# Kernel optimization log

Measured on AMD Instinct MI355X. Metric: run time of the kernel, lower is better.

The kernel has to match this reference:

```python
import jax, jax.numpy as jnp
import numpy as np

N = 100000          # nodes
E = 1600000         # directed edges (before self-loops)
F_IN = 500          # num_features
HID = 16            # hidden_dim
HEADS = 8
NUM_CLASSES = 10
NEG_SLOPE = 0.2     # PyG GATConv default
BN_EPS = 1e-5


def setup_inputs() -> dict:
    key = jax.random.key(0)
    ks = jax.random.split(key, 20)
    def glorot(k, shape):
        fan = shape[0] + shape[-1]
        return jax.random.normal(k, shape, jnp.float32) * jnp.sqrt(2.0 / fan)
    x = jax.random.normal(ks[0], (N, F_IN), jnp.float32)
    edge_index = jax.random.randint(ks[1], (2, E), 0, N, dtype=jnp.int32)
    inp = {
        'x': x, 'edge_index': edge_index,
        # conv1: F_IN -> HID, 8 heads
        'W1': glorot(ks[2], (F_IN, HEADS * HID)),
        'a1_src': glorot(ks[3], (HEADS, HID)),
        'a1_dst': glorot(ks[4], (HEADS, HID)),
        'b1': jnp.zeros((HEADS * HID,), jnp.float32),
        'g1': jnp.ones((HEADS * HID,), jnp.float32),
        'be1': jnp.zeros((HEADS * HID,), jnp.float32),
        # conv2: 128 -> HID, 8 heads
        'W2': glorot(ks[5], (HEADS * HID, HEADS * HID)),
        'a2_src': glorot(ks[6], (HEADS, HID)),
        'a2_dst': glorot(ks[7], (HEADS, HID)),
        'b2': jnp.zeros((HEADS * HID,), jnp.float32),
        'g2': jnp.ones((HEADS * HID,), jnp.float32),
        'be2': jnp.zeros((HEADS * HID,), jnp.float32),
        # conv3: 128 -> NUM_CLASSES, 1 head
        'W3': glorot(ks[8], (HEADS * HID, NUM_CLASSES)),
        'a3_src': glorot(ks[9], (1, NUM_CLASSES)),
        'a3_dst': glorot(ks[10], (1, NUM_CLASSES)),
        'b3': jnp.zeros((NUM_CLASSES,), jnp.float32),
    }
    return inp


def gat_conv(x, src, dst, W, a_src, a_dst, b, heads, out_ch):
    n = x.shape[0]
    h = (x @ W).reshape(n, heads, out_ch)                      # [N,H,C]
    al_src = jnp.einsum('nhc,hc->nh', h, a_src)                # [N,H]
    al_dst = jnp.einsum('nhc,hc->nh', h, a_dst)                # [N,H]
    e = al_src[src] + al_dst[dst]                              # [E,H]
    e = jnp.where(e > 0, e, NEG_SLOPE * e)                     # LeakyReLU
    # segment softmax over incoming edges of each dst node
    m = jax.ops.segment_max(e, dst, num_segments=n)            # [N,H]
    m = jnp.where(jnp.isfinite(m), m, 0.0)
    p = jnp.exp(e - m[dst])                                    # [E,H]
    denom = jax.ops.segment_sum(p, dst, num_segments=n)        # [N,H]
    alpha = p / jnp.maximum(denom[dst], 1e-16)                 # [E,H]
    msg = h[src] * alpha[:, :, None]                           # [E,H,C]
    out = jax.ops.segment_sum(msg, dst, num_segments=n)        # [N,H,C]
    return out.reshape(n, heads * out_ch) + b


def batch_norm_eval(x, gamma, beta):
    # eval-mode BN with running_mean=0, running_var=1
    return x * (gamma / jnp.sqrt(1.0 + BN_EPS)) + beta


def reference(x, edge_index, W1, a1_src, a1_dst, b1, g1, be1,
              W2, a2_src, a2_dst, b2, g2, be2,
              W3, a3_src, a3_dst, b3):
    loops = jnp.arange(N, dtype=edge_index.dtype)
    src = jnp.concatenate([edge_index[0], loops])
    dst = jnp.concatenate([edge_index[1], loops])
    h = jax.nn.elu(gat_conv(x, src, dst, W1, a1_src, a1_dst, b1, HEADS, HID))
    h = batch_norm_eval(h, g1, be1)
    h = jax.nn.elu(gat_conv(h, src, dst, W2, a2_src, a2_dst, b2, HEADS, HID))
    h = batch_norm_eval(h, g2, be2)
    h = gat_conv(h, src, dst, W3, a3_src, a3_dst, b3, 1, NUM_CLASSES)
    return jax.nn.log_softmax(h, axis=1)
```

## Files before the change

kernel.cpp:

```cpp
#include <hip/hip_runtime.h>
#include <math.h>

#define N_NODES 100000
#define N_EDGES 1600000
#define ET (N_EDGES + N_NODES)
#define F_IN 500
#define D1 128
#define HEADS 8
#define HID 16
#define NCLS 10
#define MAXDEG 64
#define NB 391
#define NSUB 8
#define CAPS 1024
#define CPAD 16

using frag = __attribute__((ext_vector_type(8))) short;
using f4   = __attribute__((ext_vector_type(4))) float;

__device__ __forceinline__ unsigned short f2bf(float x) {
    unsigned u = __float_as_uint(x);
    unsigned r = u + 0x7fff + ((u >> 16) & 1);
    return (unsigned short)(r >> 16);
}
__device__ __forceinline__ unsigned short f2bf_tr(float x) {
    return (unsigned short)(__float_as_uint(x) >> 16);
}
__device__ __forceinline__ float bf2f(unsigned short b) {
    return __uint_as_float(((unsigned)b) << 16);
}
__device__ __forceinline__ float bflo(unsigned u) { return __uint_as_float(u << 16); }
__device__ __forceinline__ float bfhi(unsigned u) { return __uint_as_float(u & 0xffff0000u); }
__device__ __forceinline__ float lrelu(float e) { return (e > 0.f) ? e : 0.2f * e; }

__global__ __launch_bounds__(256) void k_bin(const int* __restrict__ eidx,
                                             int* __restrict__ bincnt,
                                             int* __restrict__ bin) {
    unsigned xcc;
    asm("s_getreg_b32 %0, hwreg(HW_REG_XCC_ID)" : "=s"(xcc));
    int base = blockIdx.x * 1024 + threadIdx.x;
#pragma unroll
    for (int k = 0; k < 4; k++) {
        int i = base + k * 256;
        if (i < ET) {
            int s, d;
            if (i < N_EDGES) { s = eidx[i]; d = eidx[N_EDGES + i]; }
            else             { s = i - N_EDGES; d = s; }
            int sb = (d >> 8) * NSUB + (int)xcc;
            int pos = atomicAdd(&bincnt[sb * CPAD], 1);
            if (pos < CAPS) bin[(size_t)sb * CAPS + pos] = (s << 8) | (d & 255);
        }
    }
}

__global__ __launch_bounds__(256) void k_build(const int* __restrict__ bincnt,
                                               const int* __restrict__ bin,
                                               int* __restrict__ cnt,
                                               int* __restrict__ slots) {
    __shared__ int lcnt[256];
    __shared__ int lsl[256 * MAXDEG];
    const int b   = blockIdx.x;
    const int tid = threadIdx.x;
    lcnt[tid] = 0;
    __syncthreads();
    for (int sub = 0; sub < NSUB; sub++) {
        int sb = b * NSUB + sub;
        int len = min(bincnt[sb * CPAD], CAPS);
        const int* bp = bin + (size_t)sb * CAPS;
        for (int i = tid; i < len; i += 256) {
            int v = bp[i];
            int doff = v & 255;
            int j = atomicAdd(&lcnt[doff], 1);
            if (j < MAXDEG) lsl[doff * MAXDEG + j] = v >> 8;
        }
    }
    __syncthreads();
    int node0 = b * 256;
    int nloc = min(256, N_NODES - node0);
    if (tid < nloc) cnt[node0 + tid] = min(lcnt[tid], MAXDEG);
    int total4 = (nloc * MAXDEG) >> 2;
    int4* dst4 = (int4*)(slots + (size_t)node0 * MAXDEG);
    const int4* src4 = (const int4*)lsl;
    for (int i = tid; i < total4; i += 256) dst4[i] = src4[i];
}

template<int K, int KP>
__global__ __launch_bounds__(256) void k_pack(const float* __restrict__ W,
                                              short* __restrict__ bhi,
                                              short* __restrict__ blo) {
    int t = blockIdx.x * 256 + threadIdx.x;
    if (t >= KP * 128) return;
    int n = t & 127, k = t >> 7;
    float w = (k < K) ? W[k * 128 + n] : 0.f;
    unsigned short h = f2bf(w);
    unsigned short l = f2bf(w - bf2f(h));
    int kt = k >> 5, kq = (k >> 3) & 3, j = k & 7, nt = n >> 4;
    int lane = kq * 16 + (n & 15);
    int idx = ((kt * 8 + nt) * 64 + lane) * 8 + j;
    bhi[idx] = (short)h;
    blo[idx] = (short)l;
}

template<int K, int NSTEP>
__global__ __launch_bounds__(256, 3) void k_mfma_gemm(const float* __restrict__ A,
                                                      const short* __restrict__ Bhi,
                                                      const short* __restrict__ Blo,
                                                      unsigned* __restrict__ hb, int n) {
    __shared__ short Ah[64 * 40];
    __shared__ short Al[64 * 40];
    const int tid  = threadIdx.x;
    const int lane = tid & 63;
    const int w    = tid >> 6;
    const int wm   = w >> 1, wn = w & 1;
    const int r0   = blockIdx.x * 64;

    float4 ld[2];
    auto issue_loads = [&](int k0) {
#pragma unroll
        for (int p = 0; p < 2; p++) {
            int c = tid + p * 256;
            int row = r0 + (c >> 3);
            int kk = k0 + ((c & 7) << 2);
            if (row < n && kk < K) ld[p] = *(const float4*)(A + (size_t)row * K + kk);
            else                   ld[p] = float4{0.f, 0.f, 0.f, 0.f};
        }
    };
    auto stage = [&]() {
#pragma unroll
        for (int p = 0; p < 2; p++) {
            int c = tid + p * 256;
            int row = c >> 3;
            int kc = (c & 7) << 2;
            float4 v = ld[p];
            unsigned short h0 = f2bf(v.x), h1 = f2bf(v.y), h2 = f2bf(v.z), h3 = f2bf(v.w);
            unsigned short q0 = f2bf_tr(v.x - bf2f(h0)), q1 = f2bf_tr(v.y - bf2f(h1));
            unsigned short q2 = f2bf_tr(v.z - bf2f(h2)), q3 = f2bf_tr(v.w - bf2f(h3));
            int off = row * 40 + kc;
            *(uint2*)(&Ah[off]) = uint2{(unsigned)h0 | ((unsigned)h1 << 16),
                                        (unsigned)h2 | ((unsigned)h3 << 16)};
            *(uint2*)(&Al[off]) = uint2{(unsigned)q0 | ((unsigned)q1 << 16),
                                        (unsigned)q2 | ((unsigned)q3 << 16)};
        }
    };

    f4 acc[2][4];
#pragma unroll
    for (int a = 0; a < 2; a++)
#pragma unroll
        for (int b = 0; b < 4; b++) acc[a][b] = f4{0.f, 0.f, 0.f, 0.f};

    issue_loads(0);
    for (int s = 0; s < NSTEP; s++) {
        if (s > 0) __syncthreads();
        stage();
        if (s + 1 < NSTEP) issue_loads((s + 1) * 32);
        __syncthreads();
        frag ahi[2], alo[2];
        const int kb = (lane >> 4) * 8;
#pragma unroll
        for (int mt = 0; mt < 2; mt++) {
            int row = wm * 32 + mt * 16 + (lane & 15);
            ahi[mt] = *(const frag*)(&Ah[row * 40 + kb]);
            alo[mt] = *(const frag*)(&Al[row * 40 + kb]);
        }
#pragma unroll
        for (int nn = 0; nn < 4; nn++) {
            int nt = wn * 4 + nn;
            frag bh = *(const frag*)(Bhi + (((size_t)s * 8 + nt) * 64 + lane) * 8);
            frag bl = *(const frag*)(Blo + (((size_t)s * 8 + nt) * 64 + lane) * 8);
#pragma unroll
            for (int mt = 0; mt < 2; mt++) {
                acc[mt][nn] = __builtin_amdgcn_mfma_f32_16x16x32_bf16(ahi[mt], bh, acc[mt][nn], 0, 0, 0);
                acc[mt][nn] = __builtin_amdgcn_mfma_f32_16x16x32_bf16(ahi[mt], bl, acc[mt][nn], 0, 0, 0);
                acc[mt][nn] = __builtin_amdgcn_mfma_f32_16x16x32_bf16(alo[mt], bh, acc[mt][nn], 0, 0, 0);
            }
        }
    }

#pragma unroll
    for (int mt = 0; mt < 2; mt++) {
        int rowb = r0 + wm * 32 + mt * 16 + (lane >> 4) * 4;
#pragma unroll
        for (int nn = 0; nn < 4; nn++) {
#pragma unroll
            for (int i = 0; i < 4; i++) {
                float v  = acc[mt][nn][i];
                float v2 = __shfl_xor(v, 1);
                int row = rowb + i;
                if (!(lane & 1) && row < n) {
                    unsigned pk = (unsigned)f2bf(v) | ((unsigned)f2bf(v2) << 16);
                    hb[(size_t)row * 64 + wn * 32 + nn * 8 + ((lane & 15) >> 1)] = pk;
                }
            }
        }
    }
}

__global__ __launch_bounds__(256) void k_attn_bf(const unsigned* __restrict__ hb,
                                                 const float* __restrict__ a_src,
                                                 const float* __restrict__ a_dst,
                                                 float* __restrict__ als,
                                                 float* __restrict__ ald, int n) {
    int t = blockIdx.x * blockDim.x + threadIdx.x;
    if (t >= n * 8) return;
    int hd = t & 7;
    const unsigned* hp = hb + (size_t)(t >> 3) * 64 + hd * 8;
    uint4 ua = *(const uint4*)hp;
    uint4 ub = *(const uint4*)(hp + 4);
    unsigned uu[8] = {ua.x, ua.y, ua.z, ua.w, ub.x, ub.y, ub.z, ub.w};
    float s1 = 0.f, s2 = 0.f;
#pragma unroll
    for (int j = 0; j < 8; j++) {
        unsigned u = uu[j];
        float v0 = bflo(u), v1 = bfhi(u);
        s1 += v0 * a_src[hd * 16 + 2 * j] + v1 * a_src[hd * 16 + 2 * j + 1];
        s2 += v0 * a_dst[hd * 16 + 2 * j] + v1 * a_dst[hd * 16 + 2 * j + 1];
    }
    als[t] = s1;
    ald[t] = s2;
}

__global__ __launch_bounds__(256) void k_agg128(const unsigned* __restrict__ hb,
                                                const float* __restrict__ als,
                                                const float* __restrict__ ald,
                                                const int* __restrict__ cnt,
                                                const int* __restrict__ slots,
                                                const float* __restrict__ bias,
                                                const float* __restrict__ gamma,
                                                const float* __restrict__ beta,
                                                float* __restrict__ out, int n) {
    int lane = threadIdx.x & 63;
    int node = __builtin_amdgcn_readfirstlane(blockIdx.x * 4 + (threadIdx.x >> 6));
    if (node >= n) return;
    int head = lane >> 3;
    float aldv = ald[node * 8 + head];
    int deg = min(cnt[node], MAXDEG);
    const int* sl = slots + (long)node * MAXDEG;

    float l = 0.f, accx = 0.f, accy = 0.f;
    int j = 0;
    for (; j + 1 < deg; j += 2) {
        int s0 = sl[j], s1 = sl[j + 1];
        unsigned u0 = hb[(size_t)s0 * 64 + lane];
        unsigned u1 = hb[(size_t)s1 * 64 + lane];
        float p0 = __expf(lrelu(als[s0 * 8 + head] + aldv));
        float p1 = __expf(lrelu(als[s1 * 8 + head] + aldv));
        l += p0 + p1;
        accx += p0 * bflo(u0) + p1 * bflo(u1);
        accy += p0 * bfhi(u0) + p1 * bfhi(u1);
    }
    if (j < deg) {
        int s0 = sl[j];
        unsigned u0 = hb[(size_t)s0 * 64 + lane];
        float p0 = __expf(lrelu(als[s0 * 8 + head] + aldv));
        l += p0;
        accx += p0 * bflo(u0);
        accy += p0 * bfhi(u0);
    }
    float inv = 1.f / fmaxf(l, 1e-16f);
    const float bnr = rsqrtf(1.0f + 1e-5f);
    int c0 = 2 * lane;
    float v0 = accx * inv + bias[c0];
    v0 = (v0 > 0.f) ? v0 : expm1f(v0);
    v0 = v0 * (gamma[c0] * bnr) + beta[c0];
    float v1 = accy * inv + bias[c0 + 1];
    v1 = (v1 > 0.f) ? v1 : expm1f(v1);
    v1 = v1 * (gamma[c0 + 1] * bnr) + beta[c0 + 1];
    out[(long)node * 128 + c0]     = v0;
    out[(long)node * 128 + c0 + 1] = v1;
}

__global__ __launch_bounds__(256) void k_gemm_w3(const float* __restrict__ A,
                                                 const float* __restrict__ W,
                                                 const float* __restrict__ a_src,
                                                 const float* __restrict__ a_dst,
                                                 float* __restrict__ out,
                                                 float* __restrict__ als,
                                                 float* __restrict__ ald, int n) {
    __shared__ float w[D1 * NCLS];
    for (int idx = threadIdx.x; idx < D1 * NCLS; idx += 256) w[idx] = W[idx];
    __syncthreads();
    int node = blockIdx.x * 256 + threadIdx.x;
    if (node >= n) return;
    const float* ar = A + (long)node * D1;
    float acc[NCLS];
#pragma unroll
    for (int cc = 0; cc < NCLS; cc++) acc[cc] = 0.f;
    for (int k = 0; k < D1; k++) {
        float av = ar[k];
#pragma unroll
        for (int cc = 0; cc < NCLS; cc++) acc[cc] = fmaf(av, w[k * NCLS + cc], acc[cc]);
    }
    float s1 = 0.f, s2 = 0.f;
#pragma unroll
    for (int cc = 0; cc < NCLS; cc++) {
        out[(long)node * NCLS + cc] = acc[cc];
        s1 += acc[cc] * a_src[cc];
        s2 += acc[cc] * a_dst[cc];
    }
    als[node] = s1;
    ald[node] = s2;
}

__global__ __launch_bounds__(256) void k_agg3(const float* __restrict__ h3,
                                              const float* __restrict__ als,
                                              const float* __restrict__ ald,
                                              const int* __restrict__ cnt,
                                              const int* __restrict__ slots,
                                              const float* __restrict__ b3,
                                              float* __restrict__ out, int n) {
    int lane = threadIdx.x & 63;
    int node = __builtin_amdgcn_readfirstlane(blockIdx.x * 4 + (threadIdx.x >> 6));
    if (node >= n) return;
    int g = lane >> 4, r = lane & 15;
    float aldv = ald[node];
    int deg = min(cnt[node], MAXDEG);
    const int* sl = slots + (long)node * MAXDEG;

    float l = 0.f, acc = 0.f;
    for (int j = g; j < deg; j += 4) {
        int s = sl[j];
        float p = __expf(lrelu(als[s] + aldv));
        l += p;
        acc += p * ((r < NCLS) ? h3[(long)s * NCLS + r] : 0.f);
    }
    l   += __shfl_xor(l, 16);   l   += __shfl_xor(l, 32);
    acc += __shfl_xor(acc, 16); acc += __shfl_xor(acc, 32);

    float z = acc / fmaxf(l, 1e-16f) + ((r < NCLS) ? b3[r] : 0.f);
    float zm = (r < NCLS) ? z : -INFINITY;
#pragma unroll
    for (int off = 8; off > 0; off >>= 1) zm = fmaxf(zm, __shfl_xor(zm, off));
    float pe = (r < NCLS) ? __expf(z - zm) : 0.f;
#pragma unroll
    for (int off = 8; off > 0; off >>= 1) pe += __shfl_xor(pe, off);
    if (g == 0 && r < NCLS) out[(long)node * NCLS + r] = z - zm - logf(pe);
}

extern "C" void kernel_launch(void* const* d_in, const int* in_sizes, int n_in,
                              void* d_out, int out_size, void* d_ws, size_t ws_size,
                              hipStream_t stream) {
    const float* x   = (const float*)d_in[0];
    const int*   eix = (const int*)  d_in[1];
    const float* W1  = (const float*)d_in[2];
    const float* a1s = (const float*)d_in[3];
    const float* a1d = (const float*)d_in[4];
    const float* b1  = (const float*)d_in[5];
    const float* g1  = (const float*)d_in[6];
    const float* be1 = (const float*)d_in[7];
    const float* W2  = (const float*)d_in[8];
    const float* a2s = (const float*)d_in[9];
    const float* a2d = (const float*)d_in[10];
    const float* b2  = (const float*)d_in[11];
    const float* g2  = (const float*)d_in[12];
    const float* be2 = (const float*)d_in[13];
    const float* W3  = (const float*)d_in[14];
    const float* a3s = (const float*)d_in[15];
    const float* a3d = (const float*)d_in[16];
    const float* b3  = (const float*)d_in[17];
    float* out = (float*)d_out;

    unsigned* hb  = (unsigned*)d_ws;
    float* feat   = (float*)(hb + (size_t)N_NODES * 64);
    float* h3     = feat + (size_t)N_NODES * 128;
    float* als    = h3   + (size_t)N_NODES * 16;
    float* ald    = als  + (size_t)N_NODES * HEADS;
    int*   cnt    = (int*)(ald + (size_t)N_NODES * HEADS);
    int*   slots  = cnt + (size_t)N_NODES;
    short* b1hi   = (short*)(slots + (size_t)N_NODES * MAXDEG);
    short* b1lo   = b1hi + 512 * 128;
    short* b2hi   = b1lo + 512 * 128;
    short* b2lo   = b2hi + 128 * 128;

    int* bincnt = (int*)feat;
    int* bin    = bincnt + (size_t)NB * NSUB * CPAD;

    hipMemsetAsync(bincnt, 0, (size_t)NB * NSUB * CPAD * sizeof(int), stream);
    k_bin<<<(ET + 1023) / 1024, 256, 0, stream>>>(eix, bincnt, bin);
    k_build<<<NB, 256, 0, stream>>>(bincnt, bin, cnt, slots);
    k_pack<F_IN, 512><<<(512 * 128 + 255) / 256, 256, 0, stream>>>(W1, b1hi, b1lo);
    k_pack<D1, 128><<<(128 * 128 + 255) / 256, 256, 0, stream>>>(W2, b2hi, b2lo);

    const int gemm_grid = (N_NODES + 63) / 64;

    k_mfma_gemm<F_IN, 16><<<gemm_grid, 256, 0, stream>>>(x, b1hi, b1lo, hb, N_NODES);
    k_attn_bf<<<(N_NODES * 8 + 255) / 256, 256, 0, stream>>>(hb, a1s, a1d, als, ald, N_NODES);
    k_agg128<<<(N_NODES + 3) / 4, 256, 0, stream>>>(hb, als, ald, cnt, slots, b1, g1, be1, feat, N_NODES);

    k_mfma_gemm<D1, 4><<<gemm_grid, 256, 0, stream>>>(feat, b2hi, b2lo, hb, N_NODES);
    k_attn_bf<<<(N_NODES * 8 + 255) / 256, 256, 0, stream>>>(hb, a2s, a2d, als, ald, N_NODES);
    k_agg128<<<(N_NODES + 3) / 4, 256, 0, stream>>>(hb, als, ald, cnt, slots, b2, g2, be2, feat, N_NODES);

    k_gemm_w3<<<(N_NODES + 255) / 256, 256, 0, stream>>>(feat, W3, a3s, a3d, h3, als, ald, N_NODES);
    k_agg3<<<(N_NODES + 3) / 4, 256, 0, stream>>>(h3, als, ald, cnt, slots, b3, out, N_NODES);
}
```

Before: 769.7 us.

## Stream GEMM A tiles into double-buffered LDS via async global-to-LDS loads

The MFMA GEMM now copies fp32 A tiles straight from global memory into a double-buffered, XOR-swizzled LDS array with global_load_lds. Each next tile is prefetched while the current one is computed. The bf16 hi/lo split moves from the staging step into registers after the LDS read, and the block tile grows from 64 to 128 rows, so each wave handles four M-subtiles and reuses each B fragment more. This aims to cut register staging, one barrier per step and repeated B loads, at the cost of more accumulator registers and reads past K that rely on zero-padded B rows.

```diff
diff --git a/kernel.cpp b/kernel.cpp
--- a/kernel.cpp
+++ b/kernel.cpp
@@ -106,62 +106,61 @@
                                                       const short* __restrict__ Bhi,
                                                       const short* __restrict__ Blo,
                                                       unsigned* __restrict__ hb, int n) {
-    __shared__ short Ah[64 * 40];
-    __shared__ short Al[64 * 40];
+    __shared__ float Af[2][128 * 32];
     const int tid  = threadIdx.x;
     const int lane = tid & 63;
     const int w    = tid >> 6;
     const int wm   = w >> 1, wn = w & 1;
-    const int r0   = blockIdx.x * 64;
-
-    float4 ld[2];
-    auto issue_loads = [&](int k0) {
-#pragma unroll
-        for (int p = 0; p < 2; p++) {
-            int c = tid + p * 256;
-            int row = r0 + (c >> 3);
-            int kk = k0 + ((c & 7) << 2);
-            if (row < n && kk < K) ld[p] = *(const float4*)(A + (size_t)row * K + kk);
-            else                   ld[p] = float4{0.f, 0.f, 0.f, 0.f};
+    const int r0   = blockIdx.x * 128;
+    const size_t lastf = (size_t)n * K - 4;
+
+    auto issue = [&](int s, int p) {
+        const int k0 = s * 32;
+#pragma unroll
+        for (int q = 0; q < 4; q++) {
+            int gi  = (w * 4 + q) * 64 + lane;
+            int row = gi >> 3, g = gi & 7;
+            int gsw = g ^ (row & 7);
+            size_t fidx = (size_t)(r0 + row) * K + k0 + gsw * 4;
+            if (fidx > lastf) fidx = lastf;
+            const float* gp = A + fidx;
+            const float* lp = &Af[p][(w * 4 + q) * 256];
+            __builtin_amdgcn_global_load_lds(
+                (const __attribute__((address_space(1))) void*)gp,
+                (__attribute__((address_space(3))) void*)lp, 16, 0, 0);
         }
     };
-    auto stage = [&]() {
-#pragma unroll
-        for (int p = 0; p < 2; p++) {
-            int c = tid + p * 256;
-            int row = c >> 3;
-            int kc = (c & 7) << 2;
-            float4 v = ld[p];
-            unsigned short h0 = f2bf(v.x), h1 = f2bf(v.y), h2 = f2bf(v.z), h3 = f2bf(v.w);
-            unsigned short q0 = f2bf_tr(v.x - bf2f(h0)), q1 = f2bf_tr(v.y - bf2f(h1));
-            unsigned short q2 = f2bf_tr(v.z - bf2f(h2)), q3 = f2bf_tr(v.w - bf2f(h3));
-            int off = row * 40 + kc;
-            *(uint2*)(&Ah[off]) = uint2{(unsigned)h0 | ((unsigned)h1 << 16),
-                                        (unsigned)h2 | ((unsigned)h3 << 16)};
-            *(uint2*)(&Al[off]) = uint2{(unsigned)q0 | ((unsigned)q1 << 16),
-                                        (unsigned)q2 | ((unsigned)q3 << 16)};
-        }
-    };
-
-    f4 acc[2][4];
-#pragma unroll
-    for (int a = 0; a < 2; a++)
+
+    f4 acc[4][4];
+#pragma unroll
+    for (int a = 0; a < 4; a++)
 #pragma unroll
         for (int b = 0; b < 4; b++) acc[a][b] = f4{0.f, 0.f, 0.f, 0.f};
 
-    issue_loads(0);
+    issue(0, 0);
+    int p = 0;
     for (int s = 0; s < NSTEP; s++) {
-        if (s > 0) __syncthreads();
-        stage();
-        if (s + 1 < NSTEP) issue_loads((s + 1) * 32);
         __syncthreads();
-        frag ahi[2], alo[2];
-        const int kb = (lane >> 4) * 8;
-#pragma unroll
-        for (int mt = 0; mt < 2; mt++) {
-            int row = wm * 32 + mt * 16 + (lane & 15);
-            ahi[mt] = *(const frag*)(&Ah[row * 40 + kb]);
-            alo[mt] = *(const frag*)(&Al[row * 40 + kb]);
+        if (s + 1 < NSTEP) issue(s + 1, p ^ 1);
+
+        frag ahi[4], alo[4];
+        const int g0 = (lane >> 4) * 2;
+#pragma unroll
+        for (int mt = 0; mt < 4; mt++) {
+            int row = wm * 64 + mt * 16 + (lane & 15);
+            int rb = row * 32, rs = row & 7;
+            float4 fa = *(const float4*)(&Af[p][rb + ((g0 ^ rs) << 2)]);
+            float4 fb = *(const float4*)(&Af[p][rb + (((g0 + 1) ^ rs) << 2)]);
+            float f[8] = {fa.x, fa.y, fa.z, fa.w, fb.x, fb.y, fb.z, fb.w};
+            frag h, l;
+#pragma unroll
+            for (int j = 0; j < 8; j++) {
+                unsigned short hh = f2bf(f[j]);
+                h[j] = (short)hh;
+                l[j] = (short)f2bf_tr(f[j] - bf2f(hh));
+            }
+            ahi[mt] = h;
+            alo[mt] = l;
         }
 #pragma unroll
         for (int nn = 0; nn < 4; nn++) {
@@ -169,17 +168,18 @@
             frag bh = *(const frag*)(Bhi + (((size_t)s * 8 + nt) * 64 + lane) * 8);
             frag bl = *(const frag*)(Blo + (((size_t)s * 8 + nt) * 64 + lane) * 8);
 #pragma unroll
-            for (int mt = 0; mt < 2; mt++) {
+            for (int mt = 0; mt < 4; mt++) {
                 acc[mt][nn] = __builtin_amdgcn_mfma_f32_16x16x32_bf16(ahi[mt], bh, acc[mt][nn], 0, 0, 0);
                 acc[mt][nn] = __builtin_amdgcn_mfma_f32_16x16x32_bf16(ahi[mt], bl, acc[mt][nn], 0, 0, 0);
                 acc[mt][nn] = __builtin_amdgcn_mfma_f32_16x16x32_bf16(alo[mt], bh, acc[mt][nn], 0, 0, 0);
             }
         }
-    }
-
-#pragma unroll
-    for (int mt = 0; mt < 2; mt++) {
-        int rowb = r0 + wm * 32 + mt * 16 + (lane >> 4) * 4;
+        p ^= 1;
+    }
+
+#pragma unroll
+    for (int mt = 0; mt < 4; mt++) {
+        int rowb = r0 + wm * 64 + mt * 16 + (lane >> 4) * 4;
 #pragma unroll
         for (int nn = 0; nn < 4; nn++) {
 #pragma unroll
@@ -381,7 +381,7 @@
     k_pack<F_IN, 512><<<(512 * 128 + 255) / 256, 256, 0, stream>>>(W1, b1hi, b1lo);
     k_pack<D1, 128><<<(128 * 128 + 255) / 256, 256, 0, stream>>>(W2, b2hi, b2lo);
 
-    const int gemm_grid = (N_NODES + 63) / 64;
+    const int gemm_grid = (N_NODES + 127) / 128;
 
     k_mfma_gemm<F_IN, 16><<<gemm_grid, 256, 0, stream>>>(x, b1hi, b1lo, hb, N_NODES);
     k_attn_bf<<<(N_NODES * 8 + 255) / 256, 256, 0, stream>>>(hb, a1s, a1d, als, ald, N_NODES);
```

After: 793.4 us. 3.1% more time.
